# Kernel tuning notes

Measured on AMD Instinct MI355X. Metric: run time of the kernel, lower is better.

## Reference

```python
import jax, jax.numpy as jnp
import numpy as np

N = 50000      # nodes
E = 800000     # edges (before self-loops)
IN = 128       # in_channels
HID = 16       # hidden_channels
HEADS = 8
OUT = 16       # out_channels
NEG_SLOPE = 0.2
BN_EPS = 1e-5
LN_EPS = 1e-5


def setup_inputs() -> dict:
    key = jax.random.key(0)
    ks = jax.random.split(key, 16)
    s = 0.05
    inp = {
        "x": jax.random.normal(ks[0], (N, IN), jnp.float32),
        "edge_index": jax.random.randint(ks[1], (2, E), 0, N, jnp.int64),
        # conv1 (in=IN, out=HID, heads=HEADS, concat=True)
        "Wl1": jax.random.normal(ks[2], (HEADS * HID, IN), jnp.float32) * s,
        "bl1": jnp.zeros((HEADS * HID,), jnp.float32),
        "Wr1": jax.random.normal(ks[3], (HEADS * HID, IN), jnp.float32) * s,
        "br1": jnp.zeros((HEADS * HID,), jnp.float32),
        "att1": jax.random.normal(ks[4], (HEADS, HID), jnp.float32) * s,
        "bias1": jnp.zeros((HEADS * HID,), jnp.float32),
        # batchnorm (eval mode, running stats)
        "bn_w": jnp.ones((HEADS * HID,), jnp.float32),
        "bn_b": jnp.zeros((HEADS * HID,), jnp.float32),
        "bn_rm": jnp.zeros((HEADS * HID,), jnp.float32),
        "bn_rv": jnp.ones((HEADS * HID,), jnp.float32),
        # conv2 (in=HEADS*HID, out=OUT, heads=HEADS, concat=False)
        "Wl2": jax.random.normal(ks[5], (HEADS * OUT, HEADS * HID), jnp.float32) * s,
        "bl2": jnp.zeros((HEADS * OUT,), jnp.float32),
        "Wr2": jax.random.normal(ks[6], (HEADS * OUT, HEADS * HID), jnp.float32) * s,
        "br2": jnp.zeros((HEADS * OUT,), jnp.float32),
        "att2": jax.random.normal(ks[7], (HEADS, OUT), jnp.float32) * s,
        "bias2": jnp.zeros((OUT,), jnp.float32),
        # skip + layernorm
        "Wskip": jax.random.normal(ks[8], (OUT, IN), jnp.float32) * s,
        "ln_w": jnp.ones((OUT,), jnp.float32),
        "ln_b": jnp.zeros((OUT,), jnp.float32),
    }
    return inp


def _gatv2(x, src, dst, Wl, bl, Wr, br, att, bias, heads, ch, concat):
    """PyG GATv2Conv (share_weights=False), eval mode (no dropout)."""
    n = x.shape[0]
    xl = (x @ Wl.T + bl).reshape(n, heads, ch)   # source transform
    xr = (x @ Wr.T + br).reshape(n, heads, ch)   # target transform
    # edge-wise attention score
    e = jax.nn.leaky_relu(xl[src] + xr[dst], NEG_SLOPE)          # [E',H,C]
    score = jnp.einsum('ehc,hc->eh', e, att)                      # [E',H]
    # segment softmax over incoming edges per destination node
    smax = jax.ops.segment_max(score, dst, num_segments=n)
    ex = jnp.exp(score - smax[dst])
    denom = jax.ops.segment_sum(ex, dst, num_segments=n)
    alpha = ex / denom[dst]                                       # [E',H]
    out = jax.ops.segment_sum(alpha[:, :, None] * xl[src], dst, num_segments=n)
    if concat:
        out = out.reshape(n, heads * ch)
    else:
        out = out.mean(axis=1)
    return out + bias


def reference(x, edge_index, Wl1, bl1, Wr1, br1, att1, bias1,
              bn_w, bn_b, bn_rm, bn_rv,
              Wl2, bl2, Wr2, br2, att2, bias2,
              Wskip, ln_w, ln_b):
    n = x.shape[0]
    loops = jnp.arange(n, dtype=edge_index.dtype)
    src = jnp.concatenate([edge_index[0], loops])
    dst = jnp.concatenate([edge_index[1], loops])

    x_res = x @ Wskip.T                                            # [N,OUT]

    h = _gatv2(x, src, dst, Wl1, bl1, Wr1, br1, att1, bias1, HEADS, HID, True)
    # BatchNorm1d in eval mode
    h = (h - bn_rm) * jax.lax.rsqrt(bn_rv + BN_EPS) * bn_w + bn_b
    h = jax.nn.elu(h)

    h = _gatv2(h, src, dst, Wl2, bl2, Wr2, br2, att2, bias2, HEADS, OUT, False)

    y = h + x_res
    mu = y.mean(axis=-1, keepdims=True)
    var = ((y - mu) ** 2).mean(axis=-1, keepdims=True)
    return (y - mu) * jax.lax.rsqrt(var + LN_EPS) * ln_w + ln_b
```

## Files before the change

### kernel.cpp

```cpp
#include <hip/hip_runtime.h>

#define NEG_SLOPE 0.2f
#define BN_EPS 1e-5f
#define LN_EPS 1e-5f

typedef __bf16 bf16_t;
typedef bf16_t bf16x8 __attribute__((ext_vector_type(8)));
typedef float floatx4 __attribute__((ext_vector_type(4)));

__device__ __forceinline__ unsigned short f2bf(float f) {
  unsigned u = __float_as_uint(f);
  u += 0x7FFFu + ((u >> 16) & 1u);
  return (unsigned short)(u >> 16);
}
__device__ __forceinline__ float bf_lo(unsigned u) { return __uint_as_float(u << 16); }
__device__ __forceinline__ float bf_hi(unsigned u) { return __uint_as_float(u & 0xFFFF0000u); }

__global__ void cvt_all(const float* __restrict__ x,
                        const float* __restrict__ wl1, const float* __restrict__ wr1,
                        const float* __restrict__ wl2, const float* __restrict__ wr2,
                        const float* __restrict__ wsk,
                        const float* __restrict__ bias1,
                        const float* __restrict__ bn_w, const float* __restrict__ bn_b,
                        const float* __restrict__ bn_rm, const float* __restrict__ bn_rv,
                        const int* __restrict__ ei, int E,
                        unsigned short* __restrict__ xbf,
                        unsigned short* __restrict__ wcat1,
                        unsigned short* __restrict__ wcat2,
                        int* __restrict__ deg, unsigned short* __restrict__ rpos,
                        float* __restrict__ bnS, float* __restrict__ bnT,
                        int n4x) {
  const int W4 = 128 * 128 / 4;
  const int S4 = 16 * 128 / 4;
  int i = blockIdx.x * blockDim.x + threadIdx.x;
  const float* src;
  unsigned short* dst;
  int j;
  if (i < n4x) { src = x; dst = xbf; j = i; }
  else {
    j = i - n4x;
    if (j < W4)               { src = wl1; dst = wcat1; }
    else if (j < 2 * W4)      { src = wr1; dst = wcat1 + 128 * 128; j -= W4; }
    else if (j < 3 * W4)      { src = wl2; dst = wcat2; j -= 2 * W4; }
    else if (j < 4 * W4)      { src = wr2; dst = wcat2 + 128 * 128; j -= 3 * W4; }
    else if (j < 4 * W4 + S4) { src = wsk; dst = wcat1 + 256 * 128; j -= 4 * W4; }
    else {
      j -= 4 * W4 + S4;
      if (j < 32) {
        for (int t = j * 4; t < j * 4 + 4; ++t) {
          float S = bn_w[t] * rsqrtf(bn_rv[t] + BN_EPS);
          bnS[t] = S;
          bnT[t] = (bias1[t] - bn_rm[t]) * S + bn_b[t];
        }
      } else {
        int e = j - 32;
        if (e < E) {
          int d = ei[E + e];
          rpos[e] = (unsigned short)atomicAdd(&deg[d], 1);
        }
      }
      return;
    }
  }
  float4 v = ((const float4*)src)[j];
  ushort4 o;
  o.x = f2bf(v.x); o.y = f2bf(v.y); o.z = f2bf(v.z); o.w = f2bf(v.w);
  ((ushort4*)dst)[j] = o;
}

__global__ __launch_bounds__(1024)
void scan_deg(const int* __restrict__ deg, int* __restrict__ indptr, int n) {
  __shared__ int carry;
  __shared__ int wsum[16];
  int lane = threadIdx.x & 63, wid = threadIdx.x >> 6;
  if (threadIdx.x == 0) { carry = 0; indptr[0] = 0; }
  __syncthreads();
  for (int base = 0; base < n; base += 4096) {
    int i0 = base + (int)threadIdx.x * 4;
    int4 v = make_int4(0, 0, 0, 0);
    if (i0 + 3 < n) v = *(const int4*)(deg + i0);
    else {
      if (i0 < n)     v.x = deg[i0];
      if (i0 + 1 < n) v.y = deg[i0 + 1];
      if (i0 + 2 < n) v.z = deg[i0 + 2];
      if (i0 + 3 < n) v.w = deg[i0 + 3];
    }
    v.x = (v.x + 1) & ~1; v.y = (v.y + 1) & ~1; v.z = (v.z + 1) & ~1; v.w = (v.w + 1) & ~1;
    int s1 = v.x, s2 = s1 + v.y, s3 = s2 + v.z, s4 = s3 + v.w;
    int s = s4;
#pragma unroll
    for (int d = 1; d < 64; d <<= 1) { int t = __shfl_up(s, d, 64); if (lane >= d) s += t; }
    if (lane == 63) wsum[wid] = s;
    __syncthreads();
    if (threadIdx.x < 16) {
      int ws = wsum[threadIdx.x];
#pragma unroll
      for (int d = 1; d < 16; d <<= 1) { int t = __shfl_up(ws, d, 16); if ((int)threadIdx.x >= d) ws += t; }
      wsum[threadIdx.x] = ws;
    }
    __syncthreads();
    int off = carry + (wid ? wsum[wid - 1] : 0) + (s - s4);
    if (i0 < n)     indptr[i0 + 1] = off + s1;
    if (i0 + 1 < n) indptr[i0 + 2] = off + s2;
    if (i0 + 2 < n) indptr[i0 + 3] = off + s3;
    if (i0 + 3 < n) indptr[i0 + 4] = off + s4;
    __syncthreads();
    if (threadIdx.x == 0) carry += wsum[15];
    __syncthreads();
  }
}

__global__ void scatter_edges(const int* __restrict__ ei, int E,
                              const int* __restrict__ indptr,
                              const unsigned short* __restrict__ rpos,
                              unsigned short* __restrict__ csr) {
  int e = blockIdx.x * blockDim.x + threadIdx.x;
  if (e < E) {
    int d = ei[E + e];
    csr[indptr[d] + (int)rpos[e]] = (unsigned short)ei[e];
  }
}

template <bool MIXED>
__global__ __launch_bounds__(256)
void gemm_bf16_mfma(const unsigned short* __restrict__ A, const unsigned short* __restrict__ B,
                    const float* __restrict__ bias0, const float* __restrict__ bias1,
                    unsigned short* __restrict__ Cbf, float* __restrict__ Cf,
                    int M, int pstrips) {
  int wave = (int)((blockIdx.x * blockDim.x + threadIdx.x) >> 6);
  int lane = threadIdx.x & 63;
  int mtiles = (M + 31) >> 5;
  if (wave >= mtiles * pstrips) return;
  int mt = wave % mtiles, ps = wave / mtiles;
  int r = lane & 15, quad = lane >> 4;

  const unsigned short* Abase = A + (size_t)(mt * 32 + r) * 128 + quad * 8;
  bf16x8 a0[4], a1[4];
#pragma unroll
  for (int k = 0; k < 4; ++k) {
    a0[k] = *(const bf16x8*)(Abase + 32 * k);
    a1[k] = *(const bf16x8*)(Abase + 16 * 128 + 32 * k);
  }

  int row0 = mt * 32 + quad * 4;
  const int Ptot = MIXED ? 272 : 256;
#pragma unroll
  for (int pp = 0; pp < 4; ++pp) {
    int p0 = ps * 64 + pp * 16;
    if (p0 >= Ptot) break;
    const unsigned short* Bbase = B + (size_t)(p0 + r) * 128 + quad * 8;
    bf16x8 b[4];
#pragma unroll
    for (int k = 0; k < 4; ++k) b[k] = *(const bf16x8*)(Bbase + 32 * k);
    floatx4 acc0 = {0.f, 0.f, 0.f, 0.f};
    floatx4 acc1 = {0.f, 0.f, 0.f, 0.f};
#pragma unroll
    for (int k = 0; k < 4; ++k) {
      acc0 = __builtin_amdgcn_mfma_f32_16x16x32_bf16(a0[k], b[k], acc0, 0, 0, 0);
      acc1 = __builtin_amdgcn_mfma_f32_16x16x32_bf16(a1[k], b[k], acc1, 0, 0, 0);
    }
    int col = p0 + r;
    if (MIXED && col >= 256) {
#pragma unroll
      for (int i = 0; i < 4; ++i) {
        if (row0 + i < M)      Cf[(size_t)(row0 + i) * 16 + (col - 256)] = acc0[i];
        if (row0 + 16 + i < M) Cf[(size_t)(row0 + 16 + i) * 16 + (col - 256)] = acc1[i];
      }
    } else {
      float bs = (col < 128) ? bias0[col] : bias1[col - 128];
#pragma unroll
      for (int i = 0; i < 4; ++i) {
        if (row0 + i < M)      Cbf[(size_t)(row0 + i) * 256 + col] = f2bf(acc0[i] + bs);
        if (row0 + 16 + i < M) Cbf[(size_t)(row0 + 16 + i) * 256 + col] = f2bf(acc1[i] + bs);
      }
    }
  }
}

template <int LAYER>
__global__ __launch_bounds__(256)
void gat_agg(const unsigned int* __restrict__ xlr,
             const int* __restrict__ indptr, const int* __restrict__ deg,
             const unsigned short* __restrict__ csr,
             const float* __restrict__ att,
             const float* __restrict__ p0, const float* __restrict__ p1,
             const float* __restrict__ p2, const float* __restrict__ p3,
             void* __restrict__ outp, int n, int nwaves) {
  int lane = threadIdx.x & 63;
  int gw = (int)((blockIdx.x * blockDim.x + threadIdx.x) >> 6);
  int half = lane >> 5, sl = lane & 31;
  float4 at = ((const float4*)att)[sl];
  float a0 = 0.6f * at.x, a1 = 0.6f * at.y, a2 = 0.6f * at.z, a3 = 0.6f * at.w;

  for (int dst = gw; dst < n; dst += nwaves) {
    int dsts = __builtin_amdgcn_readfirstlane(dst);
    int beg = __builtin_amdgcn_readfirstlane(indptr[dsts]);
    int dg = __builtin_amdgcn_readfirstlane(deg[dsts]);
    const unsigned* cp = (const unsigned*)csr + (beg >> 1);
    int tot = dg + 1;
    int npair = (tot + 1) >> 1;

    uint2 ur = *(const uint2*)(xlr + (size_t)dsts * 128 + 64 + sl * 2);
    float xr0 = bf_lo(ur.x), xr1 = bf_hi(ur.x), xr2 = bf_lo(ur.y), xr3 = bf_hi(ur.y);
    float lA = 0.f, lB = 0.f;
    float cA0 = 0.f, cA1 = 0.f, cA2 = 0.f, cA3 = 0.f;
    float cB0 = 0.f, cB1 = 0.f, cB2 = 0.f, cB3 = 0.f;

    for (int p = 0; p < npair; p += 4) {
      uint2 u[4];
      float vm[4];
#pragma unroll
      for (int k = 0; k < 4; ++k) {
        unsigned pr = cp[p + k];
        int e0 = 2 * (p + k), e1 = e0 + 1;
        int sA = (e0 < dg) ? (int)(pr & 0xFFFFu) : dsts;
        int sB = (e1 < dg) ? (int)(pr >> 16) : dsts;
        float mA = (e0 < tot) ? 1.f : 0.f;
        float mB = (e1 < tot) ? 1.f : 0.f;
        int s = half ? sB : sA;
        vm[k] = half ? mB : mA;
        u[k] = *(const uint2*)(xlr + ((size_t)s << 7) + sl * 2);
      }
#pragma unroll
      for (int k = 0; k < 4; ++k) {
        float x0 = bf_lo(u[k].x), x1 = bf_hi(u[k].x), x2 = bf_lo(u[k].y), x3 = bf_hi(u[k].y);
        float e0 = x0 + xr0, e1 = x1 + xr1, e2 = x2 + xr2, e3 = x3 + xr3;
        float sc = fmaf(fmaf(fabsf(e0), 0.66666667f, e0), a0,
                   fmaf(fmaf(fabsf(e1), 0.66666667f, e1), a1,
                   fmaf(fmaf(fabsf(e2), 0.66666667f, e2), a2,
                        fmaf(fabsf(e3), 0.66666667f, e3) * a3)));
        sc += __shfl_xor(sc, 1);
        sc += __shfl_xor(sc, 2);
        float pw = __expf(sc) * vm[k];
        if (k & 1) {
          lB += pw;
          cB0 = fmaf(pw, x0, cB0); cB1 = fmaf(pw, x1, cB1);
          cB2 = fmaf(pw, x2, cB2); cB3 = fmaf(pw, x3, cB3);
        } else {
          lA += pw;
          cA0 = fmaf(pw, x0, cA0); cA1 = fmaf(pw, x1, cA1);
          cA2 = fmaf(pw, x2, cA2); cA3 = fmaf(pw, x3, cA3);
        }
      }
    }
    float l = lA + lB;
    float c0 = cA0 + cB0, c1 = cA1 + cB1, c2 = cA2 + cB2, c3 = cA3 + cB3;
    l  += __shfl_xor(l, 32);
    c0 += __shfl_xor(c0, 32); c1 += __shfl_xor(c1, 32);
    c2 += __shfl_xor(c2, 32); c3 += __shfl_xor(c3, 32);
    float inv = 1.f / l;

    if (LAYER == 1) {
      float4 S = ((const float4*)p0)[sl];
      float4 T = ((const float4*)p1)[sl];
      float o0 = fmaf(c0 * inv, S.x, T.x);
      float o1 = fmaf(c1 * inv, S.y, T.y);
      float o2 = fmaf(c2 * inv, S.z, T.z);
      float o3 = fmaf(c3 * inv, S.w, T.w);
      o0 = (o0 > 0.f) ? o0 : (__expf(o0) - 1.f);
      o1 = (o1 > 0.f) ? o1 : (__expf(o1) - 1.f);
      o2 = (o2 > 0.f) ? o2 : (__expf(o2) - 1.f);
      o3 = (o3 > 0.f) ? o3 : (__expf(o3) - 1.f);
      if (half == 0) {
        uint2 o;
        o.x = ((unsigned)f2bf(o1) << 16) | f2bf(o0);
        o.y = ((unsigned)f2bf(o3) << 16) | f2bf(o2);
        ((uint2*)outp)[(size_t)dst * 32 + sl] = o;
      }
    } else {
      float y0 = c0 * inv, y1 = c1 * inv, y2 = c2 * inv, y3 = c3 * inv;
#pragma unroll
      for (int d = 4; d <= 16; d <<= 1) {
        y0 += __shfl_xor(y0, d); y1 += __shfl_xor(y1, d);
        y2 += __shfl_xor(y2, d); y3 += __shfl_xor(y3, d);
      }
      int chh = (sl & 3) * 4;
      float4 b2 = *(const float4*)(p1 + chh);
      float4 xs = *(const float4*)(p0 + (size_t)dst * 16 + chh);
      y0 = y0 * 0.125f + b2.x + xs.x;
      y1 = y1 * 0.125f + b2.y + xs.y;
      y2 = y2 * 0.125f + b2.z + xs.z;
      y3 = y3 * 0.125f + b2.w + xs.w;
      float t = (y0 + y1) + (y2 + y3);
      t += __shfl_xor(t, 1); t += __shfl_xor(t, 2);
      float mu = t * (1.f / 16.f);
      float d0 = y0 - mu, d1 = y1 - mu, d2 = y2 - mu, d3 = y3 - mu;
      float v = (d0 * d0 + d1 * d1) + (d2 * d2 + d3 * d3);
      v += __shfl_xor(v, 1); v += __shfl_xor(v, 2);
      float istd = rsqrtf(v * (1.f / 16.f) + LN_EPS);
      float4 lw = *(const float4*)(p2 + chh);
      float4 lb = *(const float4*)(p3 + chh);
      if (lane < 4) {
        float4 o;
        o.x = d0 * istd * lw.x + lb.x;
        o.y = d1 * istd * lw.y + lb.y;
        o.z = d2 * istd * lw.z + lb.z;
        o.w = d3 * istd * lw.w + lb.w;
        *(float4*)((float*)outp + (size_t)dst * 16 + chh) = o;
      }
    }
  }
}

extern "C" void kernel_launch(void* const* d_in, const int* in_sizes, int n_in,
                              void* d_out, int out_size, void* d_ws, size_t ws_size,
                              hipStream_t stream) {
  const float* x     = (const float*)d_in[0];
  const int*   ei    = (const int*)d_in[1];
  const float* Wl1   = (const float*)d_in[2];
  const float* bl1   = (const float*)d_in[3];
  const float* Wr1   = (const float*)d_in[4];
  const float* br1   = (const float*)d_in[5];
  const float* att1  = (const float*)d_in[6];
  const float* bias1 = (const float*)d_in[7];
  const float* bn_w  = (const float*)d_in[8];
  const float* bn_b  = (const float*)d_in[9];
  const float* bn_rm = (const float*)d_in[10];
  const float* bn_rv = (const float*)d_in[11];
  const float* Wl2   = (const float*)d_in[12];
  const float* bl2   = (const float*)d_in[13];
  const float* Wr2   = (const float*)d_in[14];
  const float* br2   = (const float*)d_in[15];
  const float* att2  = (const float*)d_in[16];
  const float* bias2 = (const float*)d_in[17];
  const float* Wskip = (const float*)d_in[18];
  const float* ln_w  = (const float*)d_in[19];
  const float* ln_b  = (const float*)d_in[20];

  const int N = in_sizes[0] / 128;
  const int E = in_sizes[1] / 2;

  char* w = (char*)d_ws;
  size_t off = 0;
  auto alloc = [&](size_t bytes) -> void* {
    void* p = (void*)(w + off);
    off += (bytes + 255) & ~(size_t)255;
    return p;
  };
  unsigned short* xbf    = (unsigned short*)alloc((size_t)N * 128 * 2);
  unsigned short* wcat1  = (unsigned short*)alloc(272 * 128 * 2);
  unsigned short* wcat2  = (unsigned short*)alloc(256 * 128 * 2);
  unsigned int*   xlr    = (unsigned int*)alloc((size_t)N * 128 * 4);
  float*          xres   = (float*)alloc((size_t)N * 16 * 4);
  unsigned short* hbf    = (unsigned short*)alloc((size_t)N * 128 * 2);
  float*          bnS    = (float*)alloc(128 * 4);
  float*          bnT    = (float*)alloc(128 * 4);
  int*            deg    = (int*)alloc((size_t)N * 4);
  int*            indptr = (int*)alloc((size_t)(N + 1) * 4);
  unsigned short* rpos   = (unsigned short*)alloc((size_t)E * 2);
  unsigned short* csr    = (unsigned short*)alloc((size_t)(E + N) * 2 + 256);

  hipMemsetAsync(deg, 0, (size_t)N * 4, stream);
  {
    int n4x = (N * 128) / 4;
    int tot = n4x + 4 * (128 * 128 / 4) + (16 * 128 / 4) + 32 + E;
    cvt_all<<<(tot + 255) / 256, 256, 0, stream>>>(
        x, Wl1, Wr1, Wl2, Wr2, Wskip, bias1, bn_w, bn_b, bn_rm, bn_rv, ei, E,
        xbf, wcat1, wcat2, deg, rpos, bnS, bnT, n4x);
  }

  scan_deg<<<1, 1024, 0, stream>>>(deg, indptr, N);
  scatter_edges<<<(E + 255) / 256, 256, 0, stream>>>(ei, E, indptr, rpos, csr);

  {
    int mtiles = (N + 31) >> 5;
    int waves = mtiles * 5;
    gemm_bf16_mfma<true><<<(waves + 3) / 4, 256, 0, stream>>>(
        xbf, wcat1, bl1, br1, (unsigned short*)xlr, xres, N, 5);
  }

  {
    int blocks = 2048, nwaves = blocks * 4;
    gat_agg<1><<<blocks, 256, 0, stream>>>(xlr, indptr, deg, csr, att1,
                                           bnS, bnT, nullptr, nullptr, (void*)hbf, N, nwaves);
  }

  {
    int mtiles = (N + 31) >> 5;
    int waves = mtiles * 4;
    gemm_bf16_mfma<false><<<(waves + 3) / 4, 256, 0, stream>>>(
        hbf, wcat2, bl2, br2, (unsigned short*)xlr, nullptr, N, 4);
  }

  {
    int blocks = 2048, nwaves = blocks * 4;
    gat_agg<2><<<blocks, 256, 0, stream>>>(xlr, indptr, deg, csr, att2,
                                           xres, bias2, ln_w, ln_b, d_out, N, nwaves);
  }
}
```

Measured before the change: 323.7 us.

## Coarsen edge-degree and scatter threads; vectorize GAT attention math with packed float2

Each thread in the degree-count part of cvt_all now handles 8 edges strided by ET, and each thread in scatter_edges handles 4 edges, so far fewer threads are launched for those phases. In gat_agg the score and accumulation math uses float2 vectors so the compiler can emit packed FP32 ops. The leaky-relu is rewritten as max(e, 0.2e), replacing the abs-based form with its 0.6 pre-scale of att. Fewer threads per edge means less latency hiding for the atomics and scattered stores, and the packed math only helps if the aggregation is ALU-bound.

```diff
diff --git a/kernel.cpp b/kernel.cpp
--- a/kernel.cpp
+++ b/kernel.cpp
@@ -7,6 +7,7 @@
 typedef __bf16 bf16_t;
 typedef bf16_t bf16x8 __attribute__((ext_vector_type(8)));
 typedef float floatx4 __attribute__((ext_vector_type(4)));
+typedef float floatx2 __attribute__((ext_vector_type(2)));
 
 __device__ __forceinline__ unsigned short f2bf(float f) {
   unsigned u = __float_as_uint(f);
@@ -23,7 +24,7 @@
                         const float* __restrict__ bias1,
                         const float* __restrict__ bn_w, const float* __restrict__ bn_b,
                         const float* __restrict__ bn_rm, const float* __restrict__ bn_rv,
-                        const int* __restrict__ ei, int E,
+                        const int* __restrict__ ei, int E, int ET,
                         unsigned short* __restrict__ xbf,
                         unsigned short* __restrict__ wcat1,
                         unsigned short* __restrict__ wcat2,
@@ -53,10 +54,16 @@
           bnT[t] = (bias1[t] - bn_rm[t]) * S + bn_b[t];
         }
       } else {
-        int e = j - 32;
-        if (e < E) {
-          int d = ei[E + e];
-          rpos[e] = (unsigned short)atomicAdd(&deg[d], 1);
+        int t = j - 32;
+        if (t < ET) {
+#pragma unroll
+          for (int k = 0; k < 8; ++k) {
+            int e = t + k * ET;
+            if (e < E) {
+              int d = ei[E + e];
+              rpos[e] = (unsigned short)atomicAdd(&deg[d], 1);
+            }
+          }
         }
       }
       return;
@@ -110,14 +117,19 @@
   }
 }
 
-__global__ void scatter_edges(const int* __restrict__ ei, int E,
+__global__ void scatter_edges(const int* __restrict__ ei, int E, int ST,
                               const int* __restrict__ indptr,
                               const unsigned short* __restrict__ rpos,
                               unsigned short* __restrict__ csr) {
-  int e = blockIdx.x * blockDim.x + threadIdx.x;
-  if (e < E) {
-    int d = ei[E + e];
-    csr[indptr[d] + (int)rpos[e]] = (unsigned short)ei[e];
+  int t = blockIdx.x * blockDim.x + threadIdx.x;
+  if (t >= ST) return;
+#pragma unroll
+  for (int k = 0; k < 4; ++k) {
+    int e = t + k * ST;
+    if (e < E) {
+      int d = ei[E + e];
+      csr[indptr[d] + (int)rpos[e]] = (unsigned short)ei[e];
+    }
   }
 }
 
@@ -190,7 +202,7 @@
   int gw = (int)((blockIdx.x * blockDim.x + threadIdx.x) >> 6);
   int half = lane >> 5, sl = lane & 31;
   float4 at = ((const float4*)att)[sl];
-  float a0 = 0.6f * at.x, a1 = 0.6f * at.y, a2 = 0.6f * at.z, a3 = 0.6f * at.w;
+  floatx2 a01 = {at.x, at.y}, a23 = {at.z, at.w};
 
   for (int dst = gw; dst < n; dst += nwaves) {
     int dsts = __builtin_amdgcn_readfirstlane(dst);
@@ -201,10 +213,11 @@
     int npair = (tot + 1) >> 1;
 
     uint2 ur = *(const uint2*)(xlr + (size_t)dsts * 128 + 64 + sl * 2);
-    float xr0 = bf_lo(ur.x), xr1 = bf_hi(ur.x), xr2 = bf_lo(ur.y), xr3 = bf_hi(ur.y);
+    floatx2 xr01 = {bf_lo(ur.x), bf_hi(ur.x)};
+    floatx2 xr23 = {bf_lo(ur.y), bf_hi(ur.y)};
     float lA = 0.f, lB = 0.f;
-    float cA0 = 0.f, cA1 = 0.f, cA2 = 0.f, cA3 = 0.f;
-    float cB0 = 0.f, cB1 = 0.f, cB2 = 0.f, cB3 = 0.f;
+    floatx2 cA01 = {0.f, 0.f}, cA23 = {0.f, 0.f};
+    floatx2 cB01 = {0.f, 0.f}, cB23 = {0.f, 0.f};
 
     for (int p = 0; p < npair; p += 4) {
       uint2 u[4];
@@ -223,31 +236,36 @@
       }
 #pragma unroll
       for (int k = 0; k < 4; ++k) {
-        float x0 = bf_lo(u[k].x), x1 = bf_hi(u[k].x), x2 = bf_lo(u[k].y), x3 = bf_hi(u[k].y);
-        float e0 = x0 + xr0, e1 = x1 + xr1, e2 = x2 + xr2, e3 = x3 + xr3;
-        float sc = fmaf(fmaf(fabsf(e0), 0.66666667f, e0), a0,
-                   fmaf(fmaf(fabsf(e1), 0.66666667f, e1), a1,
-                   fmaf(fmaf(fabsf(e2), 0.66666667f, e2), a2,
-                        fmaf(fabsf(e3), 0.66666667f, e3) * a3)));
+        floatx2 x01 = {bf_lo(u[k].x), bf_hi(u[k].x)};
+        floatx2 x23 = {bf_lo(u[k].y), bf_hi(u[k].y)};
+        floatx2 e01 = x01 + xr01;
+        floatx2 e23 = x23 + xr23;
+        floatx2 t01 = __builtin_elementwise_max(e01, e01 * NEG_SLOPE);
+        floatx2 t23 = __builtin_elementwise_max(e23, e23 * NEG_SLOPE);
+        floatx2 s2 = t01 * a01 + t23 * a23;
+        float sc = s2.x + s2.y;
         sc += __shfl_xor(sc, 1);
         sc += __shfl_xor(sc, 2);
         float pw = __expf(sc) * vm[k];
+        floatx2 pv = {pw, pw};
         if (k & 1) {
           lB += pw;
-          cB0 = fmaf(pw, x0, cB0); cB1 = fmaf(pw, x1, cB1);
-          cB2 = fmaf(pw, x2, cB2); cB3 = fmaf(pw, x3, cB3);
+          cB01 = x01 * pv + cB01;
+          cB23 = x23 * pv + cB23;
         } else {
           lA += pw;
-          cA0 = fmaf(pw, x0, cA0); cA1 = fmaf(pw, x1, cA1);
-          cA2 = fmaf(pw, x2, cA2); cA3 = fmaf(pw, x3, cA3);
+          cA01 = x01 * pv + cA01;
+          cA23 = x23 * pv + cA23;
         }
       }
     }
     float l = lA + lB;
-    float c0 = cA0 + cB0, c1 = cA1 + cB1, c2 = cA2 + cB2, c3 = cA3 + cB3;
-    l  += __shfl_xor(l, 32);
-    c0 += __shfl_xor(c0, 32); c1 += __shfl_xor(c1, 32);
-    c2 += __shfl_xor(c2, 32); c3 += __shfl_xor(c3, 32);
+    floatx2 c01 = cA01 + cB01, c23 = cA23 + cB23;
+    l += __shfl_xor(l, 32);
+    float c0 = c01.x + __shfl_xor(c01.x, 32);
+    float c1 = c01.y + __shfl_xor(c01.y, 32);
+    float c2 = c23.x + __shfl_xor(c23.x, 32);
+    float c3 = c23.y + __shfl_xor(c23.y, 32);
     float inv = 1.f / l;
 
     if (LAYER == 1) {
@@ -353,14 +371,18 @@
   hipMemsetAsync(deg, 0, (size_t)N * 4, stream);
   {
     int n4x = (N * 128) / 4;
-    int tot = n4x + 4 * (128 * 128 / 4) + (16 * 128 / 4) + 32 + E;
+    int ET = (E + 7) / 8;
+    int tot = n4x + 4 * (128 * 128 / 4) + (16 * 128 / 4) + 32 + ET;
     cvt_all<<<(tot + 255) / 256, 256, 0, stream>>>(
-        x, Wl1, Wr1, Wl2, Wr2, Wskip, bias1, bn_w, bn_b, bn_rm, bn_rv, ei, E,
+        x, Wl1, Wr1, Wl2, Wr2, Wskip, bias1, bn_w, bn_b, bn_rm, bn_rv, ei, E, ET,
         xbf, wcat1, wcat2, deg, rpos, bnS, bnT, n4x);
   }
 
   scan_deg<<<1, 1024, 0, stream>>>(deg, indptr, N);
-  scatter_edges<<<(E + 255) / 256, 256, 0, stream>>>(ei, E, indptr, rpos, csr);
+  {
+    int ST = (E + 3) / 4;
+    scatter_edges<<<(ST + 255) / 256, 256, 0, stream>>>(ei, E, ST, indptr, rpos, csr);
+  }
 
   {
     int mtiles = (N + 31) >> 5;
```

Measured after the change: 340.0 us. +5.0%, slower.

## Shard degree atomics into 8 copies, pack CSR metadata, unmask aggregation loop

Applied to the files above, without the earlier changes.

Degree counting now spreads atomics across 8 per-block-group counter arrays to cut contention. The scan merges them and emits packed (start, degree) metadata plus per-shard bases for the scatter. The aggregation kernel runs an unmasked main loop over full edge pairs, with one masked tail step for the self-loop and odd edge. It also folds log2(e) into the attention weights so it can use a native exp2. The cost is an 8x larger counter memset and more scan work in a single-block kernel.

```diff
diff --git a/kernel.cpp b/kernel.cpp
--- a/kernel.cpp
+++ b/kernel.cpp
@@ -3,6 +3,12 @@
 #define NEG_SLOPE 0.2f
 #define BN_EPS 1e-5f
 #define LN_EPS 1e-5f
+
+#if __has_builtin(__builtin_amdgcn_exp2f)
+#define EXP2F(x) __builtin_amdgcn_exp2f(x)
+#else
+#define EXP2F(x) exp2f(x)
+#endif
 
 typedef __bf16 bf16_t;
 typedef bf16_t bf16x8 __attribute__((ext_vector_type(8)));
@@ -27,9 +33,9 @@
                         unsigned short* __restrict__ xbf,
                         unsigned short* __restrict__ wcat1,
                         unsigned short* __restrict__ wcat2,
-                        int* __restrict__ deg, unsigned short* __restrict__ rpos,
+                        int* __restrict__ deg8, unsigned short* __restrict__ rpos,
                         float* __restrict__ bnS, float* __restrict__ bnT,
-                        int n4x) {
+                        int n4x, int N) {
   const int W4 = 128 * 128 / 4;
   const int S4 = 16 * 128 / 4;
   int i = blockIdx.x * blockDim.x + threadIdx.x;
@@ -56,7 +62,8 @@
         int e = j - 32;
         if (e < E) {
           int d = ei[E + e];
-          rpos[e] = (unsigned short)atomicAdd(&deg[d], 1);
+          int c = (int)(blockIdx.x & 7);
+          rpos[e] = (unsigned short)atomicAdd(&deg8[(size_t)c * N + d], 1);
         }
       }
       return;
@@ -69,55 +76,75 @@
 }
 
 __global__ __launch_bounds__(1024)
-void scan_deg(const int* __restrict__ deg, int* __restrict__ indptr, int n) {
+void scan_deg(const int* __restrict__ deg8, int* __restrict__ meta,
+              int* __restrict__ cbase8, int n) {
   __shared__ int carry;
   __shared__ int wsum[16];
   int lane = threadIdx.x & 63, wid = threadIdx.x >> 6;
-  if (threadIdx.x == 0) { carry = 0; indptr[0] = 0; }
+  if (threadIdx.x == 0) carry = 0;
   __syncthreads();
   for (int base = 0; base < n; base += 4096) {
     int i0 = base + (int)threadIdx.x * 4;
-    int4 v = make_int4(0, 0, 0, 0);
-    if (i0 + 3 < n) v = *(const int4*)(deg + i0);
-    else {
-      if (i0 < n)     v.x = deg[i0];
-      if (i0 + 1 < n) v.y = deg[i0 + 1];
-      if (i0 + 2 < n) v.z = deg[i0 + 2];
-      if (i0 + 3 < n) v.w = deg[i0 + 3];
-    }
-    v.x = (v.x + 1) & ~1; v.y = (v.y + 1) & ~1; v.z = (v.z + 1) & ~1; v.w = (v.w + 1) & ~1;
-    int s1 = v.x, s2 = s1 + v.y, s3 = s2 + v.z, s4 = s3 + v.w;
+    int4 v[8];
+#pragma unroll
+    for (int c = 0; c < 8; ++c) {
+      v[c] = make_int4(0, 0, 0, 0);
+      const int* p = deg8 + (size_t)c * n;
+      if (i0 + 3 < n) v[c] = *(const int4*)(p + i0);
+      else if (i0 < n) {
+        v[c].x = p[i0];
+        if (i0 + 1 < n) v[c].y = p[i0 + 1];
+        if (i0 + 2 < n) v[c].z = p[i0 + 2];
+      }
+    }
+    int4 t = make_int4(0, 0, 0, 0);
+#pragma unroll
+    for (int c = 0; c < 8; ++c) { t.x += v[c].x; t.y += v[c].y; t.z += v[c].z; t.w += v[c].w; }
+    int g1 = (t.x + 1) & ~1, g2 = (t.y + 1) & ~1, g3 = (t.z + 1) & ~1, g4 = (t.w + 1) & ~1;
+    int s1 = g1, s2 = s1 + g2, s3 = s2 + g3, s4 = s3 + g4;
     int s = s4;
 #pragma unroll
-    for (int d = 1; d < 64; d <<= 1) { int t = __shfl_up(s, d, 64); if (lane >= d) s += t; }
+    for (int d = 1; d < 64; d <<= 1) { int tt = __shfl_up(s, d, 64); if (lane >= d) s += tt; }
     if (lane == 63) wsum[wid] = s;
     __syncthreads();
     if (threadIdx.x < 16) {
       int ws = wsum[threadIdx.x];
 #pragma unroll
-      for (int d = 1; d < 16; d <<= 1) { int t = __shfl_up(ws, d, 16); if ((int)threadIdx.x >= d) ws += t; }
+      for (int d = 1; d < 16; d <<= 1) { int tt = __shfl_up(ws, d, 16); if ((int)threadIdx.x >= d) ws += tt; }
       wsum[threadIdx.x] = ws;
     }
     __syncthreads();
     int off = carry + (wid ? wsum[wid - 1] : 0) + (s - s4);
-    if (i0 < n)     indptr[i0 + 1] = off + s1;
-    if (i0 + 1 < n) indptr[i0 + 2] = off + s2;
-    if (i0 + 2 < n) indptr[i0 + 3] = off + s3;
-    if (i0 + 3 < n) indptr[i0 + 4] = off + s4;
+    int st[4] = {off, off + s1, off + s2, off + s3};
+    int tv[4] = {t.x, t.y, t.z, t.w};
+#pragma unroll
+    for (int k = 0; k < 4; ++k) {
+      if (i0 + k < n) {
+        ((int2*)meta)[i0 + k] = make_int2(st[k], tv[k]);
+        int run = st[k];
+#pragma unroll
+        for (int c = 0; c < 8; ++c) {
+          int cnt = (k == 0) ? v[c].x : (k == 1) ? v[c].y : (k == 2) ? v[c].z : v[c].w;
+          cbase8[(size_t)c * n + i0 + k] = run;
+          run += cnt;
+        }
+      }
+    }
     __syncthreads();
     if (threadIdx.x == 0) carry += wsum[15];
     __syncthreads();
   }
 }
 
-__global__ void scatter_edges(const int* __restrict__ ei, int E,
-                              const int* __restrict__ indptr,
+__global__ void scatter_edges(const int* __restrict__ ei, int E, int ebase,
+                              const int* __restrict__ cbase8,
                               const unsigned short* __restrict__ rpos,
-                              unsigned short* __restrict__ csr) {
+                              unsigned short* __restrict__ csr, int N) {
   int e = blockIdx.x * blockDim.x + threadIdx.x;
   if (e < E) {
     int d = ei[E + e];
-    csr[indptr[d] + (int)rpos[e]] = (unsigned short)ei[e];
+    int c = ((ebase + e) >> 8) & 7;
+    csr[cbase8[(size_t)c * N + d] + (int)rpos[e]] = (unsigned short)ei[e];
   }
 }
 
@@ -180,7 +207,7 @@
 template <int LAYER>
 __global__ __launch_bounds__(256)
 void gat_agg(const unsigned int* __restrict__ xlr,
-             const int* __restrict__ indptr, const int* __restrict__ deg,
+             const int* __restrict__ meta,
              const unsigned short* __restrict__ csr,
              const float* __restrict__ att,
              const float* __restrict__ p0, const float* __restrict__ p1,
@@ -190,15 +217,15 @@
   int gw = (int)((blockIdx.x * blockDim.x + threadIdx.x) >> 6);
   int half = lane >> 5, sl = lane & 31;
   float4 at = ((const float4*)att)[sl];
-  float a0 = 0.6f * at.x, a1 = 0.6f * at.y, a2 = 0.6f * at.z, a3 = 0.6f * at.w;
+  const float SC = 0.6f * 1.44269504f;
+  float a0 = SC * at.x, a1 = SC * at.y, a2 = SC * at.z, a3 = SC * at.w;
 
   for (int dst = gw; dst < n; dst += nwaves) {
     int dsts = __builtin_amdgcn_readfirstlane(dst);
-    int beg = __builtin_amdgcn_readfirstlane(indptr[dsts]);
-    int dg = __builtin_amdgcn_readfirstlane(deg[dsts]);
+    int2 m = *(const int2*)(meta + 2 * (size_t)dsts);
+    int beg = __builtin_amdgcn_readfirstlane(m.x);
+    int dg  = __builtin_amdgcn_readfirstlane(m.y);
     const unsigned* cp = (const unsigned*)csr + (beg >> 1);
-    int tot = dg + 1;
-    int npair = (tot + 1) >> 1;
 
     uint2 ur = *(const uint2*)(xlr + (size_t)dsts * 128 + 64 + sl * 2);
     float xr0 = bf_lo(ur.x), xr1 = bf_hi(ur.x), xr2 = bf_lo(ur.y), xr3 = bf_hi(ur.y);
@@ -206,43 +233,57 @@
     float cA0 = 0.f, cA1 = 0.f, cA2 = 0.f, cA3 = 0.f;
     float cB0 = 0.f, cB1 = 0.f, cB2 = 0.f, cB3 = 0.f;
 
-    for (int p = 0; p < npair; p += 4) {
+    auto body = [&](uint2 u, float vm, bool useB, bool masked) {
+      float x0 = bf_lo(u.x), x1 = bf_hi(u.x), x2 = bf_lo(u.y), x3 = bf_hi(u.y);
+      float e0 = x0 + xr0, e1 = x1 + xr1, e2 = x2 + xr2, e3 = x3 + xr3;
+      float sc = fmaf(fmaf(fabsf(e0), 0.66666667f, e0), a0,
+                 fmaf(fmaf(fabsf(e1), 0.66666667f, e1), a1,
+                 fmaf(fmaf(fabsf(e2), 0.66666667f, e2), a2,
+                      fmaf(fabsf(e3), 0.66666667f, e3) * a3)));
+      sc += __shfl_xor(sc, 1);
+      sc += __shfl_xor(sc, 2);
+      float pw = EXP2F(sc);
+      if (masked) pw *= vm;
+      if (useB) {
+        lB += pw;
+        cB0 = fmaf(pw, x0, cB0); cB1 = fmaf(pw, x1, cB1);
+        cB2 = fmaf(pw, x2, cB2); cB3 = fmaf(pw, x3, cB3);
+      } else {
+        lA += pw;
+        cA0 = fmaf(pw, x0, cA0); cA1 = fmaf(pw, x1, cA1);
+        cA2 = fmaf(pw, x2, cA2); cA3 = fmaf(pw, x3, cA3);
+      }
+    };
+
+    int npm = dg >> 1;
+    int p = 0;
+    for (; p + 4 <= npm; p += 4) {
       uint2 u[4];
-      float vm[4];
 #pragma unroll
       for (int k = 0; k < 4; ++k) {
         unsigned pr = cp[p + k];
-        int e0 = 2 * (p + k), e1 = e0 + 1;
-        int sA = (e0 < dg) ? (int)(pr & 0xFFFFu) : dsts;
-        int sB = (e1 < dg) ? (int)(pr >> 16) : dsts;
-        float mA = (e0 < tot) ? 1.f : 0.f;
-        float mB = (e1 < tot) ? 1.f : 0.f;
-        int s = half ? sB : sA;
-        vm[k] = half ? mB : mA;
+        int s = half ? (int)(pr >> 16) : (int)(pr & 0xFFFFu);
         u[k] = *(const uint2*)(xlr + ((size_t)s << 7) + sl * 2);
       }
 #pragma unroll
-      for (int k = 0; k < 4; ++k) {
-        float x0 = bf_lo(u[k].x), x1 = bf_hi(u[k].x), x2 = bf_lo(u[k].y), x3 = bf_hi(u[k].y);
-        float e0 = x0 + xr0, e1 = x1 + xr1, e2 = x2 + xr2, e3 = x3 + xr3;
-        float sc = fmaf(fmaf(fabsf(e0), 0.66666667f, e0), a0,
-                   fmaf(fmaf(fabsf(e1), 0.66666667f, e1), a1,
-                   fmaf(fmaf(fabsf(e2), 0.66666667f, e2), a2,
-                        fmaf(fabsf(e3), 0.66666667f, e3) * a3)));
-        sc += __shfl_xor(sc, 1);
-        sc += __shfl_xor(sc, 2);
-        float pw = __expf(sc) * vm[k];
-        if (k & 1) {
-          lB += pw;
-          cB0 = fmaf(pw, x0, cB0); cB1 = fmaf(pw, x1, cB1);
-          cB2 = fmaf(pw, x2, cB2); cB3 = fmaf(pw, x3, cB3);
-        } else {
-          lA += pw;
-          cA0 = fmaf(pw, x0, cA0); cA1 = fmaf(pw, x1, cA1);
-          cA2 = fmaf(pw, x2, cA2); cA3 = fmaf(pw, x3, cA3);
-        }
-      }
-    }
+      for (int k = 0; k < 4; ++k) body(u[k], 1.f, k & 1, false);
+    }
+    for (; p < npm; ++p) {
+      unsigned pr = cp[p];
+      int s = half ? (int)(pr >> 16) : (int)(pr & 0xFFFFu);
+      uint2 u = *(const uint2*)(xlr + ((size_t)s << 7) + sl * 2);
+      body(u, 1.f, false, false);
+    }
+    {
+      unsigned pr = cp[npm];
+      int odd = dg & 1;
+      int sR = odd ? (int)(pr & 0xFFFFu) : dsts;
+      int s = half ? dsts : sR;
+      float vm = (half && !odd) ? 0.f : 1.f;
+      uint2 u = *(const uint2*)(xlr + ((size_t)s << 7) + sl * 2);
+      body(u, vm, true, true);
+    }
+
     float l = lA + lB;
     float c0 = cA0 + cB0, c1 = cA1 + cB1, c2 = cA2 + cB2, c3 = cA3 + cB3;
     l  += __shfl_xor(l, 32);
@@ -345,22 +386,26 @@
   unsigned short* hbf    = (unsigned short*)alloc((size_t)N * 128 * 2);
   float*          bnS    = (float*)alloc(128 * 4);
   float*          bnT    = (float*)alloc(128 * 4);
-  int*            deg    = (int*)alloc((size_t)N * 4);
-  int*            indptr = (int*)alloc((size_t)(N + 1) * 4);
+  int*            deg8   = (int*)alloc((size_t)8 * N * 4);
+  int*            cbase8 = (int*)alloc((size_t)8 * N * 4);
+  int*            meta   = (int*)alloc((size_t)2 * N * 4);
   unsigned short* rpos   = (unsigned short*)alloc((size_t)E * 2);
   unsigned short* csr    = (unsigned short*)alloc((size_t)(E + N) * 2 + 256);
 
-  hipMemsetAsync(deg, 0, (size_t)N * 4, stream);
+  const int n4x = (N * 128) / 4;
+  const int W4 = 128 * 128 / 4, S4 = 16 * 128 / 4;
+  const int ebase = n4x + 4 * W4 + S4 + 32;
+
+  hipMemsetAsync(deg8, 0, (size_t)8 * N * 4, stream);
   {
-    int n4x = (N * 128) / 4;
-    int tot = n4x + 4 * (128 * 128 / 4) + (16 * 128 / 4) + 32 + E;
+    int tot = ebase + E;
     cvt_all<<<(tot + 255) / 256, 256, 0, stream>>>(
         x, Wl1, Wr1, Wl2, Wr2, Wskip, bias1, bn_w, bn_b, bn_rm, bn_rv, ei, E,
-        xbf, wcat1, wcat2, deg, rpos, bnS, bnT, n4x);
-  }
-
-  scan_deg<<<1, 1024, 0, stream>>>(deg, indptr, N);
-  scatter_edges<<<(E + 255) / 256, 256, 0, stream>>>(ei, E, indptr, rpos, csr);
+        xbf, wcat1, wcat2, deg8, rpos, bnS, bnT, n4x, N);
+  }
+
+  scan_deg<<<1, 1024, 0, stream>>>(deg8, meta, cbase8, N);
+  scatter_edges<<<(E + 255) / 256, 256, 0, stream>>>(ei, E, ebase, cbase8, rpos, csr, N);
 
   {
     int mtiles = (N + 31) >> 5;
@@ -371,7 +416,7 @@
 
   {
     int blocks = 2048, nwaves = blocks * 4;
-    gat_agg<1><<<blocks, 256, 0, stream>>>(xlr, indptr, deg, csr, att1,
+    gat_agg<1><<<blocks, 256, 0, stream>>>(xlr, meta, csr, att1,
                                            bnS, bnT, nullptr, nullptr, (void*)hbf, N, nwaves);
   }
 
@@ -384,7 +429,7 @@
 
   {
     int blocks = 2048, nwaves = blocks * 4;
-    gat_agg<2><<<blocks, 256, 0, stream>>>(xlr, indptr, deg, csr, att2,
+    gat_agg<2><<<blocks, 256, 0, stream>>>(xlr, meta, csr, att2,
                                            xres, bias2, ln_w, ln_b, d_out, N, nwaves);
   }
 }
```

After: 425.2 us. 1.31x slower.
